# Performance work log

Measured on AMD Instinct MI355X. Metric: run time of the kernel, lower is better.

Reference implementation:

```python
import jax, jax.numpy as jnp
import numpy as np

T, B, D, H = 2048, 32, 512, 512

def setup_inputs() -> dict:
    key = jax.random.key(0)
    ks = jax.random.split(key, 7)
    stdv = 1.0 / np.sqrt(H)
    return {
        "x": jax.random.normal(ks[0], (T, B, D), dtype=jnp.float32),
        "h0": jax.random.normal(ks[1], (B, H), dtype=jnp.float32),
        "c0": jax.random.normal(ks[2], (B, H), dtype=jnp.float32),
        "w_ih": jax.random.uniform(ks[3], (4 * H, D), jnp.float32, -stdv, stdv),
        "b_ih": jax.random.uniform(ks[4], (4 * H,), jnp.float32, -stdv, stdv),
        "w_hh": jax.random.uniform(ks[5], (4 * H, H), jnp.float32, -stdv, stdv),
        "b_hh": jax.random.uniform(ks[6], (4 * H,), jnp.float32, -stdv, stdv),
    }

def reference(x, h0, c0, w_ih, b_ih, w_hh, b_hh):
    hidden = h0.shape[-1]
    # Precompute input-to-hidden projection for all timesteps: [T, B, 4H]
    gx = jnp.einsum("tbd,gd->tbg", x, w_ih) + b_ih + b_hh

    def step(carry, gx_t):
        h, c = carry
        gates = gx_t + h @ w_hh.T  # [B, 4H]
        i_in, f_in, g_in, o_in = jnp.split(gates, 4, axis=1)
        i_t = jax.nn.sigmoid(i_in)
        f_t = jax.nn.sigmoid(f_in)
        g_t = jnp.tanh(g_in)
        o_t = jax.nn.sigmoid(o_in)
        c_t = f_t * c + i_t * g_t
        h_t = o_t * jnp.tanh(c_t)
        return (h_t, c_t), h_t

    (h_n, c_n), out = jax.lax.scan(step, (h0, c0), gx)
    # out: [T, B, H]; matches DPLSTM output, (h_n, c_n)
    return out, h_n, c_n
```

## Files before the change

kernel.cpp:

```cpp
#include <hip/hip_runtime.h>
#include <hip/hip_bf16.h>

#define T_STEPS 2048
#define BATCH 32
#define DIN 512
#define HID 512
#define G4H 2048
#define NWG 64
#define SLICE 8
#define THREADS 256

typedef __attribute__((ext_vector_type(8))) short short8;
typedef __attribute__((ext_vector_type(4))) float floatx4;
typedef unsigned long long ull;

__device__ __forceinline__ ushort f2bf(float f) {
  return __builtin_bit_cast(ushort, __float2bfloat16(f));
}

__global__ void prep_kernel(const float* __restrict__ wih, const float* __restrict__ whh,
                            const float* __restrict__ bih, const float* __restrict__ bhh,
                            const float* __restrict__ h0,
                            ushort* __restrict__ wihb, ushort* __restrict__ whhb,
                            float* __restrict__ bias, ushort* __restrict__ hbuf,
                            unsigned* __restrict__ flags) {
  int i = blockIdx.x * blockDim.x + threadIdx.x;
  const int NW = G4H * DIN;
  if (i < NW) { wihb[i] = f2bf(wih[i]); whhb[i] = f2bf(whh[i]); }
  if (i < G4H) bias[i] = bih[i] + bhh[i];
  if (i < BATCH * HID) hbuf[i] = f2bf(h0[i]);
  if (i < 4 * NWG) flags[i] = 0u;
}

__global__ void cvtx_kernel(const float* __restrict__ x, ushort* __restrict__ xb) {
  const size_t N = (size_t)T_STEPS * BATCH * DIN;
  size_t stride = (size_t)gridDim.x * blockDim.x * 4;
  for (size_t idx = ((size_t)blockIdx.x * blockDim.x + threadIdx.x) * 4; idx < N; idx += stride) {
    float4 f = *reinterpret_cast<const float4*>(x + idx);
    ushort4 u;
    u.x = f2bf(f.x); u.y = f2bf(f.y); u.z = f2bf(f.z); u.w = f2bf(f.w);
    *reinterpret_cast<ushort4*>(xb + idx) = u;
  }
}

template <bool XB>
__device__ __forceinline__ floatx4 xpart(const float* __restrict__ x,
                                         const ushort* __restrict__ xb,
                                         int t, int brow, int quad,
                                         const short8* wih_r) {
  floatx4 acc = {0.f, 0.f, 0.f, 0.f};
  if (XB) {
    const ushort* xt = xb + ((size_t)t * BATCH + brow) * DIN + quad * 8;
#pragma unroll
    for (int kb = 0; kb < 16; ++kb) {
      short8 a0 = *reinterpret_cast<const short8*>(xt + kb * 32);
      acc = __builtin_amdgcn_mfma_f32_16x16x32_bf16(a0, wih_r[kb], acc, 0, 0, 0);
    }
  } else {
    const float* xt = x + ((size_t)t * BATCH + brow) * DIN + quad * 8;
#pragma unroll
    for (int kb = 0; kb < 16; ++kb) {
      const float4* xp = reinterpret_cast<const float4*>(xt + kb * 32);
      float4 f0 = xp[0], f1 = xp[1];
      short8 a0;
      a0[0] = (short)f2bf(f0.x); a0[1] = (short)f2bf(f0.y);
      a0[2] = (short)f2bf(f0.z); a0[3] = (short)f2bf(f0.w);
      a0[4] = (short)f2bf(f1.x); a0[5] = (short)f2bf(f1.y);
      a0[6] = (short)f2bf(f1.z); a0[7] = (short)f2bf(f1.w);
      acc = __builtin_amdgcn_mfma_f32_16x16x32_bf16(a0, wih_r[kb], acc, 0, 0, 0);
    }
  }
  return acc;
}

template <bool XB>
__global__ __launch_bounds__(THREADS, 1) void lstm_kernel(
    const float* __restrict__ x, const ushort* __restrict__ xb,
    const float* __restrict__ c0,
    const ushort* __restrict__ wihb, const ushort* __restrict__ whhb,
    const float* __restrict__ bias, ushort* __restrict__ hbuf,
    float* __restrict__ out, unsigned* __restrict__ flags) {
  const int g = blockIdx.x;
  const int tid = threadIdx.x;
  const int lane = tid & 63;
  const int wave = tid >> 6;
  const int r = wave & 1;
  const int cc = wave >> 1;
  const int n16 = lane & 15;
  const int quad = lane >> 4;
  const int brow = r * 16 + n16;

  const int j = cc * 16 + n16;
  const int wrow = (j & 3) * HID + g * SLICE + (j >> 2);

  const int eb = tid >> 3;
  const int ekk = tid & 7;
  const int ecol = g * SLICE + ekk;
  float c_val = c0[eb * HID + ecol];
  const float bi = bias[ecol];
  const float bf_ = bias[HID + ecol];
  const float bg = bias[2 * HID + ecol];
  const float bo = bias[3 * HID + ecol];

  short8 wih_r[16], whh_r[16];
  {
    const ushort* wr = wihb + (size_t)wrow * DIN + quad * 8;
    const ushort* hr = whhb + (size_t)wrow * HID + quad * 8;
#pragma unroll
    for (int kb = 0; kb < 16; ++kb) {
      wih_r[kb] = *reinterpret_cast<const short8*>(wr + kb * 32);
      whh_r[kb] = *reinterpret_cast<const short8*>(hr + kb * 32);
    }
  }

  __shared__ float gsm[2][32][33];

  floatx4 acc0_cur = xpart<XB>(x, xb, 0, brow, quad, wih_r);

  float hlast = 0.f;
  for (int t = 0; t < T_STEPS; ++t) {
    const int par = t & 1;
    if (t) {
      const ull* fp = reinterpret_cast<const ull*>(flags) + 2 * lane;
      const unsigned tgt = (unsigned)t;
      for (;;) {
        ull a = __hip_atomic_load(fp, __ATOMIC_RELAXED, __HIP_MEMORY_SCOPE_AGENT);
        ull b = __hip_atomic_load(fp + 1, __ATOMIC_RELAXED, __HIP_MEMORY_SCOPE_AGENT);
        unsigned t0 = (unsigned)a, t1 = (unsigned)(a >> 32);
        unsigned t2 = (unsigned)b, t3 = (unsigned)(b >> 32);
        unsigned mn = t0 < t1 ? t0 : t1;
        unsigned mn2 = t2 < t3 ? t2 : t3;
        if (mn2 < mn) mn = mn2;
        if (__all(mn >= tgt)) break;
        __builtin_amdgcn_s_sleep(1);
      }
    }
    __atomic_signal_fence(__ATOMIC_SEQ_CST);

    const ull* hp = reinterpret_cast<const ull*>(
        hbuf + (size_t)par * (BATCH * HID) + brow * HID + quad * 8);
    ull hl[32];
#pragma unroll
    for (int kb = 0; kb < 16; ++kb) {
      hl[2 * kb]     = __hip_atomic_load(hp + kb * 8,     __ATOMIC_RELAXED, __HIP_MEMORY_SCOPE_AGENT);
      hl[2 * kb + 1] = __hip_atomic_load(hp + kb * 8 + 1, __ATOMIC_RELAXED, __HIP_MEMORY_SCOPE_AGENT);
    }

    const int tt = (t + 1 < T_STEPS) ? t + 1 : t;
    floatx4 acc0_next = xpart<XB>(x, xb, tt, brow, quad, wih_r);

    floatx4 acc1 = {0.f, 0.f, 0.f, 0.f};
#pragma unroll
    for (int kb = 0; kb < 16; ++kb) {
      union { ull u[2]; short8 s; } cv;
      cv.u[0] = hl[2 * kb];
      cv.u[1] = hl[2 * kb + 1];
      acc1 = __builtin_amdgcn_mfma_f32_16x16x32_bf16(cv.s, whh_r[kb], acc1, 0, 0, 0);
    }

#pragma unroll
    for (int rg = 0; rg < 4; ++rg) {
      gsm[par][r * 16 + quad * 4 + rg][cc * 16 + n16] = acc0_cur[rg] + acc1[rg];
    }
    __syncthreads();

    float pi = gsm[par][eb][ekk * 4 + 0] + bi;
    float pf = gsm[par][eb][ekk * 4 + 1] + bf_;
    float pg = gsm[par][eb][ekk * 4 + 2] + bg;
    float po = gsm[par][eb][ekk * 4 + 3] + bo;
    float ig = 1.f / (1.f + __expf(-pi));
    float fg = 1.f / (1.f + __expf(-pf));
    float eg = __expf(2.f * pg);
    float gg = 1.f - 2.f / (eg + 1.f);
    float og = 1.f / (1.f + __expf(-po));
    c_val = fg * c_val + ig * gg;
    float ec = __expf(2.f * c_val);
    float tc = 1.f - 2.f / (ec + 1.f);
    float h = og * tc;
    hlast = h;
    out[(size_t)t * (BATCH * HID) + eb * HID + ecol] = h;

    int m = (int)f2bf(h) & 0xffff;
    int p0 = __shfl(m, lane & ~1);
    int p1 = __shfl(m, (lane & ~1) | 1);
    int u32v = p0 | (p1 << 16);
    int q0 = __shfl(u32v, lane & ~3);
    int q2 = __shfl(u32v, (lane & ~3) | 2);
    ull v64 = ((ull)(unsigned)q0) | (((ull)(unsigned)q2) << 32);
    if ((lane & 3) == 0) {
      int p = lane >> 2;
      int idx = (wave * 8 + (p >> 1)) * HID + g * SLICE + (p & 1) * 4;
      ull* dst = reinterpret_cast<ull*>(hbuf + (size_t)(par ^ 1) * (BATCH * HID) + idx);
      __hip_atomic_store(dst, v64, __ATOMIC_RELAXED, __HIP_MEMORY_SCOPE_AGENT);
    }
    __atomic_signal_fence(__ATOMIC_SEQ_CST);
    __builtin_amdgcn_s_waitcnt(0);
    __atomic_signal_fence(__ATOMIC_SEQ_CST);
    if (lane == 0) {
      __hip_atomic_store(&flags[g * 4 + wave], (unsigned)(t + 1),
                         __ATOMIC_RELAXED, __HIP_MEMORY_SCOPE_AGENT);
    }
    acc0_cur = acc0_next;
  }
  out[(size_t)T_STEPS * BATCH * HID + eb * HID + ecol] = hlast;
  out[(size_t)T_STEPS * BATCH * HID + BATCH * HID + eb * HID + ecol] = c_val;
}

extern "C" void kernel_launch(void* const* d_in, const int* in_sizes, int n_in,
                              void* d_out, int out_size, void* d_ws, size_t ws_size,
                              hipStream_t stream) {
  const float* x = (const float*)d_in[0];
  const float* h0 = (const float*)d_in[1];
  const float* c0 = (const float*)d_in[2];
  const float* w_ih = (const float*)d_in[3];
  const float* b_ih = (const float*)d_in[4];
  const float* w_hh = (const float*)d_in[5];
  const float* b_hh = (const float*)d_in[6];
  float* out = (float*)d_out;
  char* ws = (char*)d_ws;

  unsigned* flags = (unsigned*)ws;
  float* bias = (float*)(ws + 1024);
  ushort* wihb = (ushort*)(ws + (16 << 10));
  ushort* whhb = (ushort*)(ws + (16 << 10) + (2 << 20));
  ushort* hbuf = (ushort*)(ws + (16 << 10) + (4 << 20));
  ushort* xb = (ushort*)(ws + (8 << 20));
  const size_t xb_bytes = (size_t)T_STEPS * BATCH * DIN * sizeof(ushort);
  const bool use_xb = ws_size >= ((size_t)(8 << 20) + xb_bytes);

  hipLaunchKernelGGL(prep_kernel, dim3(4096), dim3(256), 0, stream,
                     w_ih, w_hh, b_ih, b_hh, h0, wihb, whhb, bias, hbuf, flags);

  if (use_xb) {
    hipLaunchKernelGGL(cvtx_kernel, dim3(8192), dim3(256), 0, stream, x, xb);
    void* args[] = {(void*)&x, (void*)&xb, (void*)&c0, (void*)&wihb, (void*)&whhb,
                    (void*)&bias, (void*)&hbuf, (void*)&out, (void*)&flags};
    hipLaunchCooperativeKernel(reinterpret_cast<void*>(&lstm_kernel<true>),
                               dim3(NWG), dim3(THREADS), args, 0, stream);
  } else {
    void* args[] = {(void*)&x, (void*)&xb, (void*)&c0, (void*)&wihb, (void*)&whhb,
                    (void*)&bias, (void*)&hbuf, (void*)&out, (void*)&flags};
    hipLaunchCooperativeKernel(reinterpret_cast<void*>(&lstm_kernel<false>),
                               dim3(NWG), dim3(THREADS), args, 0, stream);
  }
}
```

Baseline: 20.63 ms.

## Replace flag barrier with per-element tagged hidden-state words and swapped MFMA layout

Each hidden-state pair is packed into a 64-bit word together with its timestep tag, so consumers poll the data directly and issue MFMAs on chunks as they become valid. This replaces the separate per-wave flag array and the waitcnt-then-flag publish. The MFMA operands are swapped so each lane holds all four gates for one hidden unit, which removes the shared-memory transpose and the __syncthreads. The x-projection for the next step now runs after the cell update instead of overlapping the wait. The trade-off is twice the bytes per hidden exchange and a polling loop that may reissue loads repeatedly.

```diff
diff --git a/kernel.cpp b/kernel.cpp
--- a/kernel.cpp
+++ b/kernel.cpp
@@ -9,9 +9,11 @@
 #define NWG 64
 #define SLICE 8
 #define THREADS 256
+#define HPAIRS (BATCH * HID / 2)
 
 typedef __attribute__((ext_vector_type(8))) short short8;
 typedef __attribute__((ext_vector_type(4))) float floatx4;
+typedef __attribute__((ext_vector_type(4))) unsigned int uintx4;
 typedef unsigned long long ull;
 
 __device__ __forceinline__ ushort f2bf(float f) {
@@ -22,14 +24,18 @@
                             const float* __restrict__ bih, const float* __restrict__ bhh,
                             const float* __restrict__ h0,
                             ushort* __restrict__ wihb, ushort* __restrict__ whhb,
-                            float* __restrict__ bias, ushort* __restrict__ hbuf,
-                            unsigned* __restrict__ flags) {
+                            float* __restrict__ bias, ull* __restrict__ tagbuf) {
   int i = blockIdx.x * blockDim.x + threadIdx.x;
   const int NW = G4H * DIN;
   if (i < NW) { wihb[i] = f2bf(wih[i]); whhb[i] = f2bf(whh[i]); }
   if (i < G4H) bias[i] = bih[i] + bhh[i];
-  if (i < BATCH * HID) hbuf[i] = f2bf(h0[i]);
-  if (i < 4 * NWG) flags[i] = 0u;
+  if (i < HPAIRS) {
+    int b = i >> 8, p = i & 255;
+    ull ev = (ull)f2bf(h0[b * HID + 2 * p]);
+    ull od = (ull)f2bf(h0[b * HID + 2 * p + 1]);
+    tagbuf[i] = (od << 48) | (ev << 32);
+    tagbuf[HPAIRS + i] = 0xFFFFFFFFull;
+  }
 }
 
 __global__ void cvtx_kernel(const float* __restrict__ x, ushort* __restrict__ xb) {
@@ -48,13 +54,17 @@
                                          const ushort* __restrict__ xb,
                                          int t, int brow, int quad,
                                          const short8* wih_r) {
-  floatx4 acc = {0.f, 0.f, 0.f, 0.f};
+  floatx4 a = {0.f, 0.f, 0.f, 0.f};
+  floatx4 b = {0.f, 0.f, 0.f, 0.f};
   if (XB) {
     const ushort* xt = xb + ((size_t)t * BATCH + brow) * DIN + quad * 8;
 #pragma unroll
     for (int kb = 0; kb < 16; ++kb) {
       short8 a0 = *reinterpret_cast<const short8*>(xt + kb * 32);
-      acc = __builtin_amdgcn_mfma_f32_16x16x32_bf16(a0, wih_r[kb], acc, 0, 0, 0);
+      if (kb & 1)
+        b = __builtin_amdgcn_mfma_f32_16x16x32_bf16(wih_r[kb], a0, b, 0, 0, 0);
+      else
+        a = __builtin_amdgcn_mfma_f32_16x16x32_bf16(wih_r[kb], a0, a, 0, 0, 0);
     }
   } else {
     const float* xt = x + ((size_t)t * BATCH + brow) * DIN + quad * 8;
@@ -67,10 +77,13 @@
       a0[2] = (short)f2bf(f0.z); a0[3] = (short)f2bf(f0.w);
       a0[4] = (short)f2bf(f1.x); a0[5] = (short)f2bf(f1.y);
       a0[6] = (short)f2bf(f1.z); a0[7] = (short)f2bf(f1.w);
-      acc = __builtin_amdgcn_mfma_f32_16x16x32_bf16(a0, wih_r[kb], acc, 0, 0, 0);
-    }
-  }
-  return acc;
+      if (kb & 1)
+        b = __builtin_amdgcn_mfma_f32_16x16x32_bf16(wih_r[kb], a0, b, 0, 0, 0);
+      else
+        a = __builtin_amdgcn_mfma_f32_16x16x32_bf16(wih_r[kb], a0, a, 0, 0, 0);
+    }
+  }
+  return a + b;
 }
 
 template <bool XB>
@@ -78,8 +91,8 @@
     const float* __restrict__ x, const ushort* __restrict__ xb,
     const float* __restrict__ c0,
     const ushort* __restrict__ wihb, const ushort* __restrict__ whhb,
-    const float* __restrict__ bias, ushort* __restrict__ hbuf,
-    float* __restrict__ out, unsigned* __restrict__ flags) {
+    const float* __restrict__ bias, ull* __restrict__ tagbuf,
+    float* __restrict__ out) {
   const int g = blockIdx.x;
   const int tid = threadIdx.x;
   const int lane = tid & 63;
@@ -89,14 +102,11 @@
   const int n16 = lane & 15;
   const int quad = lane >> 4;
   const int brow = r * 16 + n16;
-
   const int j = cc * 16 + n16;
   const int wrow = (j & 3) * HID + g * SLICE + (j >> 2);
 
-  const int eb = tid >> 3;
-  const int ekk = tid & 7;
-  const int ecol = g * SLICE + ekk;
-  float c_val = c0[eb * HID + ecol];
+  const int ecol = g * SLICE + cc * 4 + quad;
+  float c_val = c0[brow * HID + ecol];
   const float bi = bias[ecol];
   const float bf_ = bias[HID + ecol];
   const float bg = bias[2 * HID + ecol];
@@ -113,61 +123,54 @@
     }
   }
 
-  __shared__ float gsm[2][32][33];
-
   floatx4 acc0_cur = xpart<XB>(x, xb, 0, brow, quad, wih_r);
 
   float hlast = 0.f;
   for (int t = 0; t < T_STEPS; ++t) {
-    const int par = t & 1;
-    if (t) {
-      const ull* fp = reinterpret_cast<const ull*>(flags) + 2 * lane;
-      const unsigned tgt = (unsigned)t;
-      for (;;) {
-        ull a = __hip_atomic_load(fp, __ATOMIC_RELAXED, __HIP_MEMORY_SCOPE_AGENT);
-        ull b = __hip_atomic_load(fp + 1, __ATOMIC_RELAXED, __HIP_MEMORY_SCOPE_AGENT);
-        unsigned t0 = (unsigned)a, t1 = (unsigned)(a >> 32);
-        unsigned t2 = (unsigned)b, t3 = (unsigned)(b >> 32);
-        unsigned mn = t0 < t1 ? t0 : t1;
-        unsigned mn2 = t2 < t3 ? t2 : t3;
-        if (mn2 < mn) mn = mn2;
-        if (__all(mn >= tgt)) break;
-        __builtin_amdgcn_s_sleep(1);
+    const ull* hb = tagbuf + (size_t)(t & 1) * HPAIRS + (size_t)brow * (HID / 2) + quad * 4;
+    const unsigned tagt = (unsigned)t;
+    floatx4 acc1a = {0.f, 0.f, 0.f, 0.f};
+    floatx4 acc1b = {0.f, 0.f, 0.f, 0.f};
+    unsigned done = 0;
+    for (;;) {
+      ull d[16][4];
+#pragma unroll
+      for (int kb = 0; kb < 16; ++kb) {
+        if (!(done & (1u << kb))) {
+#pragma unroll
+          for (int m = 0; m < 4; ++m)
+            d[kb][m] = __hip_atomic_load(hb + kb * 16 + m, __ATOMIC_RELAXED,
+                                         __HIP_MEMORY_SCOPE_AGENT);
+        }
       }
-    }
-    __atomic_signal_fence(__ATOMIC_SEQ_CST);
-
-    const ull* hp = reinterpret_cast<const ull*>(
-        hbuf + (size_t)par * (BATCH * HID) + brow * HID + quad * 8);
-    ull hl[32];
-#pragma unroll
-    for (int kb = 0; kb < 16; ++kb) {
-      hl[2 * kb]     = __hip_atomic_load(hp + kb * 8,     __ATOMIC_RELAXED, __HIP_MEMORY_SCOPE_AGENT);
-      hl[2 * kb + 1] = __hip_atomic_load(hp + kb * 8 + 1, __ATOMIC_RELAXED, __HIP_MEMORY_SCOPE_AGENT);
-    }
-
-    const int tt = (t + 1 < T_STEPS) ? t + 1 : t;
-    floatx4 acc0_next = xpart<XB>(x, xb, tt, brow, quad, wih_r);
-
-    floatx4 acc1 = {0.f, 0.f, 0.f, 0.f};
-#pragma unroll
-    for (int kb = 0; kb < 16; ++kb) {
-      union { ull u[2]; short8 s; } cv;
-      cv.u[0] = hl[2 * kb];
-      cv.u[1] = hl[2 * kb + 1];
-      acc1 = __builtin_amdgcn_mfma_f32_16x16x32_bf16(cv.s, whh_r[kb], acc1, 0, 0, 0);
-    }
-
-#pragma unroll
-    for (int rg = 0; rg < 4; ++rg) {
-      gsm[par][r * 16 + quad * 4 + rg][cc * 16 + n16] = acc0_cur[rg] + acc1[rg];
-    }
-    __syncthreads();
-
-    float pi = gsm[par][eb][ekk * 4 + 0] + bi;
-    float pf = gsm[par][eb][ekk * 4 + 1] + bf_;
-    float pg = gsm[par][eb][ekk * 4 + 2] + bg;
-    float po = gsm[par][eb][ekk * 4 + 3] + bo;
+#pragma unroll
+      for (int kb = 0; kb < 16; ++kb) {
+        if (!(done & (1u << kb))) {
+          bool ok = ((unsigned)d[kb][0] == tagt) & ((unsigned)d[kb][1] == tagt) &
+                    ((unsigned)d[kb][2] == tagt) & ((unsigned)d[kb][3] == tagt);
+          if (__all(ok)) {
+            uintx4 pk;
+            pk.x = (unsigned)(d[kb][0] >> 32);
+            pk.y = (unsigned)(d[kb][1] >> 32);
+            pk.z = (unsigned)(d[kb][2] >> 32);
+            pk.w = (unsigned)(d[kb][3] >> 32);
+            short8 hf = __builtin_bit_cast(short8, pk);
+            if (kb & 1)
+              acc1b = __builtin_amdgcn_mfma_f32_16x16x32_bf16(whh_r[kb], hf, acc1b, 0, 0, 0);
+            else
+              acc1a = __builtin_amdgcn_mfma_f32_16x16x32_bf16(whh_r[kb], hf, acc1a, 0, 0, 0);
+            done |= (1u << kb);
+          }
+        }
+      }
+      if (done == 0xFFFFu) break;
+      __builtin_amdgcn_s_sleep(1);
+    }
+
+    float pi = acc0_cur[0] + acc1a[0] + acc1b[0] + bi;
+    float pf = acc0_cur[1] + acc1a[1] + acc1b[1] + bf_;
+    float pg = acc0_cur[2] + acc1a[2] + acc1b[2] + bg;
+    float po = acc0_cur[3] + acc1a[3] + acc1b[3] + bo;
     float ig = 1.f / (1.f + __expf(-pi));
     float fg = 1.f / (1.f + __expf(-pf));
     float eg = __expf(2.f * pg);
@@ -178,32 +181,31 @@
     float tc = 1.f - 2.f / (ec + 1.f);
     float h = og * tc;
     hlast = h;
-    out[(size_t)t * (BATCH * HID) + eb * HID + ecol] = h;
-
-    int m = (int)f2bf(h) & 0xffff;
-    int p0 = __shfl(m, lane & ~1);
-    int p1 = __shfl(m, (lane & ~1) | 1);
-    int u32v = p0 | (p1 << 16);
-    int q0 = __shfl(u32v, lane & ~3);
-    int q2 = __shfl(u32v, (lane & ~3) | 2);
-    ull v64 = ((ull)(unsigned)q0) | (((ull)(unsigned)q2) << 32);
-    if ((lane & 3) == 0) {
-      int p = lane >> 2;
-      int idx = (wave * 8 + (p >> 1)) * HID + g * SLICE + (p & 1) * 4;
-      ull* dst = reinterpret_cast<ull*>(hbuf + (size_t)(par ^ 1) * (BATCH * HID) + idx);
-      __hip_atomic_store(dst, v64, __ATOMIC_RELAXED, __HIP_MEMORY_SCOPE_AGENT);
+
+    unsigned hu = (unsigned)f2bf(h);
+    unsigned hpart = (unsigned)__shfl_xor((int)hu, 16);
+    if ((quad & 1) == 0) {
+      ull v = ((ull)hpart << 48) | ((ull)hu << 32) | (ull)(unsigned)(t + 1);
+      ull* dst = tagbuf + (size_t)((t + 1) & 1) * HPAIRS +
+                 (size_t)brow * (HID / 2) + (ecol >> 1);
+      __hip_atomic_store(dst, v, __ATOMIC_RELAXED, __HIP_MEMORY_SCOPE_AGENT);
     }
     __atomic_signal_fence(__ATOMIC_SEQ_CST);
-    __builtin_amdgcn_s_waitcnt(0);
-    __atomic_signal_fence(__ATOMIC_SEQ_CST);
-    if (lane == 0) {
-      __hip_atomic_store(&flags[g * 4 + wave], (unsigned)(t + 1),
-                         __ATOMIC_RELAXED, __HIP_MEMORY_SCOPE_AGENT);
-    }
-    acc0_cur = acc0_next;
-  }
-  out[(size_t)T_STEPS * BATCH * HID + eb * HID + ecol] = hlast;
-  out[(size_t)T_STEPS * BATCH * HID + BATCH * HID + eb * HID + ecol] = c_val;
+
+    float h1 = __shfl_xor(h, 16);
+    float h2 = __shfl_xor(h, 32);
+    float h3 = __shfl_xor(h1, 32);
+    if (quad == 0) {
+      float4 o4 = make_float4(h, h1, h2, h3);
+      *reinterpret_cast<float4*>(out + (size_t)t * (BATCH * HID) + brow * HID +
+                                 g * SLICE + cc * 4) = o4;
+    }
+
+    const int tt = (t + 1 < T_STEPS) ? t + 1 : t;
+    acc0_cur = xpart<XB>(x, xb, tt, brow, quad, wih_r);
+  }
+  out[(size_t)T_STEPS * BATCH * HID + brow * HID + ecol] = hlast;
+  out[(size_t)T_STEPS * BATCH * HID + BATCH * HID + brow * HID + ecol] = c_val;
 }
 
 extern "C" void kernel_launch(void* const* d_in, const int* in_sizes, int n_in,
@@ -219,28 +221,37 @@
   float* out = (float*)d_out;
   char* ws = (char*)d_ws;
 
-  unsigned* flags = (unsigned*)ws;
   float* bias = (float*)(ws + 1024);
   ushort* wihb = (ushort*)(ws + (16 << 10));
   ushort* whhb = (ushort*)(ws + (16 << 10) + (2 << 20));
-  ushort* hbuf = (ushort*)(ws + (16 << 10) + (4 << 20));
+  ull* tagbuf = (ull*)(ws + (16 << 10) + (4 << 20));
   ushort* xb = (ushort*)(ws + (8 << 20));
   const size_t xb_bytes = (size_t)T_STEPS * BATCH * DIN * sizeof(ushort);
   const bool use_xb = ws_size >= ((size_t)(8 << 20) + xb_bytes);
 
   hipLaunchKernelGGL(prep_kernel, dim3(4096), dim3(256), 0, stream,
-                     w_ih, w_hh, b_ih, b_hh, h0, wihb, whhb, bias, hbuf, flags);
+                     w_ih, w_hh, b_ih, b_hh, h0, wihb, whhb, bias, tagbuf);
 
   if (use_xb) {
     hipLaunchKernelGGL(cvtx_kernel, dim3(8192), dim3(256), 0, stream, x, xb);
     void* args[] = {(void*)&x, (void*)&xb, (void*)&c0, (void*)&wihb, (void*)&whhb,
-                    (void*)&bias, (void*)&hbuf, (void*)&out, (void*)&flags};
-    hipLaunchCooperativeKernel(reinterpret_cast<void*>(&lstm_kernel<true>),
-                               dim3(NWG), dim3(THREADS), args, 0, stream);
+                    (void*)&bias, (void*)&tagbuf, (void*)&out};
+    hipError_t e = hipLaunchCooperativeKernel(
+        reinterpret_cast<void*>(&lstm_kernel<true>), dim3(NWG), dim3(THREADS),
+        args, 0, stream);
+    if (e != hipSuccess) {
+      hipLaunchKernelGGL(lstm_kernel<true>, dim3(NWG), dim3(THREADS), 0, stream,
+                         x, xb, c0, wihb, whhb, bias, tagbuf, out);
+    }
   } else {
     void* args[] = {(void*)&x, (void*)&xb, (void*)&c0, (void*)&wihb, (void*)&whhb,
-                    (void*)&bias, (void*)&hbuf, (void*)&out, (void*)&flags};
-    hipLaunchCooperativeKernel(reinterpret_cast<void*>(&lstm_kernel<false>),
-                               dim3(NWG), dim3(THREADS), args, 0, stream);
-  }
-}
+                    (void*)&bias, (void*)&tagbuf, (void*)&out};
+    hipError_t e = hipLaunchCooperativeKernel(
+        reinterpret_cast<void*>(&lstm_kernel<false>), dim3(NWG), dim3(THREADS),
+        args, 0, stream);
+    if (e != hipSuccess) {
+      hipLaunchKernelGGL(lstm_kernel<false>, dim3(NWG), dim3(THREADS), 0, stream,
+                         x, xb, c0, wihb, whhb, bias, tagbuf, out);
+    }
+  }
+}
```

Result: slower. 23.06 ms (+11.8%).
